# Optimization experiments

Measured on AMD Instinct MI355X. Metric: run time of the kernel, lower is better.

The kernel has to match this reference:

```python
import jax, jax.numpy as jnp
import numpy as np

N, D, H, DATT, C, NCLS = 20000, 1024, 512, 256, 10, 4

def setup_inputs() -> dict:
    key = jax.random.key(0)
    ks = jax.random.split(key, 20)
    s = lambda fan_in: 1.0 / np.sqrt(fan_in)
    u = lambda k, shape, fan_in: jax.random.uniform(k, shape, jnp.float32, -s(fan_in), s(fan_in))
    inp = {
        'x': jax.random.normal(ks[0], (N, D), jnp.float32),
        'cluster_id': jax.random.randint(ks[1], (N,), 0, C),
        # per-cluster expert MLP (phi_i): Linear(D,H)+ReLU, Linear(H,H)+ReLU (dropout=identity in eval)
        'W1': u(ks[2], (C, D, H), D), 'b1': u(ks[3], (C, H), D),
        'W2': u(ks[4], (C, H, H), H), 'b2': u(ks[5], (C, H), H),
        # attention_net: Linear(H,H)+ReLU then gated attention (L=H, D=DATT, n_classes=1)
        'fc_W': u(ks[6], (H, H), H), 'fc_b': u(ks[7], (H,), H),
        'Wa': u(ks[8], (H, DATT), H), 'ba': u(ks[9], (DATT,), H),
        'Wb': u(ks[10], (H, DATT), H), 'bb': u(ks[11], (DATT,), H),
        'Wc': u(ks[12], (DATT, 1), DATT), 'bc': u(ks[13], (1,), DATT),
        # rho: Linear(H, DATT)+ReLU
        'rho_W': u(ks[14], (H, DATT), H), 'rho_b': u(ks[15], (DATT,), H),
        # classifier
        'cls_W': u(ks[16], (DATT, NCLS), DATT), 'cls_b': u(ks[17], (NCLS,), DATT),
    }
    return inp

def reference(x, cluster_id, W1, b1, W2, b2, fc_W, fc_b, Wa, ba, Wb, bb, Wc, bc, rho_W, rho_b, cls_W, cls_b):
    # --- per-cluster expert MLPs, vectorized over clusters (no python loop over data) ---
    # h1: [C, N, H] = ReLU(x @ W1_c + b1_c) for every cluster c
    h1 = jax.nn.relu(jnp.einsum('nd,cdh->cnh', x, W1) + b1[:, None, :])
    h2 = jax.nn.relu(jnp.einsum('cnh,chk->cnk', h1, W2) + b2[:, None, :])
    # masked mean-pool per cluster (AdaptiveAvgPool1d(1) over the cluster's tokens)
    mask = (cluster_id[None, :] == jnp.arange(C)[:, None]).astype(h2.dtype)  # [C, N]
    counts = jnp.maximum(mask.sum(axis=1), 1.0)                               # empty cluster -> zeros
    h_cluster = jnp.einsum('cn,cnh->ch', mask, h2) / counts[:, None]          # [C, H]
    # --- attention net: fc + gated attention ---
    h = jax.nn.relu(h_cluster @ fc_W + fc_b)                                  # [C, H]
    a = jnp.tanh(h @ Wa + ba)
    b = jax.nn.sigmoid(h @ Wb + bb)
    A = ((a * b) @ Wc + bc).T                                                 # [1, C]
    A = jax.nn.softmax(A, axis=1)
    h_path = A @ h                                                            # [1, H]
    hr = jax.nn.relu(h_path @ rho_W + rho_b)[0]                               # [DATT] (squeeze)
    logits = (hr @ cls_W + cls_b)[None, :]                                    # [1, NCLS]
    Y_prob = jax.nn.softmax(logits, axis=1)
    Y_hat = jnp.argmax(logits, axis=1, keepdims=True)
    return (logits, Y_prob, Y_hat)
```

## Files before the change

### kernel.cpp

```cpp
#include <hip/hip_runtime.h>
#include <hip/hip_bf16.h>
#include <stdint.h>

#define NT 20000
#define DIM 1024
#define HID 512
#define DATT_N 256
#define NCLUS 10
#define NCLS_N 4
#define NRT 157
#define NBS 79

typedef __bf16 bf16;
typedef __attribute__((ext_vector_type(8))) __bf16 bf16x8;
typedef __attribute__((ext_vector_type(4))) float f32x4;

__device__ __forceinline__ void gload_lds16(const void* g, void* l) {
  __builtin_amdgcn_global_load_lds(
      (const __attribute__((address_space(1))) unsigned int*)g,
      (__attribute__((address_space(3))) unsigned int*)l, 16, 0, 0);
}


__global__ void zero_pool(float* pool) {
  int i = blockIdx.x * 256 + threadIdx.x;
  if (i < NCLUS * HID) pool[i] = 0.f;
}

__global__ __launch_bounds__(256) void hist_kernel(const int* __restrict__ cid,
                                                   int* __restrict__ blkcnt) {
  __shared__ int wcnt[4][16];
  int tid = threadIdx.x;
  int lane = tid & 63, w = tid >> 6;
  int n = blockIdx.x * 256 + tid;
  int mycid = (n < NT) ? cid[n] : -1;
#pragma unroll
  for (int c = 0; c < NCLUS; ++c) {
    unsigned long long m = __ballot(mycid == c);
    if (lane == c) wcnt[w][c] = __popcll(m);
  }
  __syncthreads();
  if (tid < NCLUS)
    blkcnt[blockIdx.x * NCLUS + tid] =
        wcnt[0][tid] + wcnt[1][tid] + wcnt[2][tid] + wcnt[3][tid];
}

__global__ void prefix_kernel(const int* __restrict__ blkcnt, int* __restrict__ blkbase,
                              int* __restrict__ cnt, int* __restrict__ offs) {
  int c = threadIdx.x;
  if (c < NCLUS) {
    int run = 0;
    for (int b = 0; b < NBS; ++b) {
      blkbase[b * NCLUS + c] = run;
      run += blkcnt[b * NCLUS + c];
    }
    cnt[c] = run;
  }
  __syncthreads();
  if (c == 0) {
    int a = 0;
    for (int i = 0; i < NCLUS; ++i) { offs[i] = a; a += cnt[i]; }
    offs[NCLUS] = a;
  }
}

__global__ __launch_bounds__(256) void scatter2_kernel(
    const int* __restrict__ cid, const int* __restrict__ blkbase,
    const int* __restrict__ offs, int* __restrict__ order) {
  __shared__ int wcnt[4][16];
  __shared__ int wbase[4][16];
  int tid = threadIdx.x;
  int lane = tid & 63, w = tid >> 6;
  int n = blockIdx.x * 256 + tid;
  int mycid = (n < NT) ? cid[n] : -1;
  unsigned long long lmask = (lane == 63) ? ~0ull >> 1 : (1ull << lane) - 1;
  int myrank = 0;
#pragma unroll
  for (int c = 0; c < NCLUS; ++c) {
    unsigned long long m = __ballot(mycid == c);
    if (mycid == c) myrank = __popcll(m & lmask);
    if (lane == c) wcnt[w][c] = __popcll(m);
  }
  __syncthreads();
  if (tid < NCLUS) {
    int pre = blkbase[blockIdx.x * NCLUS + tid];
#pragma unroll
    for (int ww = 0; ww < 4; ++ww) { wbase[ww][tid] = pre; pre += wcnt[ww][tid]; }
  }
  __syncthreads();
  if (n < NT) order[offs[mycid] + wbase[w][mycid] + myrank] = n;
}

__global__ void gather_cast(const float* __restrict__ x, const int* __restrict__ order,
                            bf16* __restrict__ xs) {
  int t = blockIdx.x * 256 + threadIdx.x;
  int row = t >> 7;
  if (row >= NT) return;
  int col = (t & 127) << 3;
  const f32x4* p = (const f32x4*)(x + (size_t)order[row] * DIM + col);
  f32x4 u = p[0], v = p[1];
  bf16x8 w;
  w[0] = (bf16)u[0]; w[1] = (bf16)u[1]; w[2] = (bf16)u[2]; w[3] = (bf16)u[3];
  w[4] = (bf16)v[0]; w[5] = (bf16)v[1]; w[6] = (bf16)v[2]; w[7] = (bf16)v[3];
  *(bf16x8*)(xs + (size_t)row * DIM + col) = w;
}

__global__ void transpose_cast(const float* __restrict__ src, bf16* __restrict__ dst,
                               int R, int Cc) {
  __shared__ float t[32][33];
  int b = blockIdx.z;
  int i0 = blockIdx.y * 32, j0 = blockIdx.x * 32;
  const float* s = src + (size_t)b * R * Cc;
  bf16* d = dst + (size_t)b * R * Cc;
  int tx = threadIdx.x & 31, ty = threadIdx.x >> 5;
#pragma unroll
  for (int yy = 0; yy < 32; yy += 8)
    t[ty + yy][tx] = s[(size_t)(i0 + ty + yy) * Cc + (j0 + tx)];
  __syncthreads();
#pragma unroll
  for (int yy = 0; yy < 32; yy += 8)
    d[(size_t)(j0 + ty + yy) * R + (i0 + tx)] = (bf16)t[tx][ty + yy];
}

__device__ __forceinline__ bool decode_grp(int d, int& c, int& rt, int& j) {
  int x8 = d & 7, s = d >> 3;
  int g = (s >> 2) * 8 + x8;
  if (g >= NRT * NCLUS) return false;
  j = s & 3;
  c = g / NRT;
  rt = g - c * NRT;
  return true;
}


__global__ __launch_bounds__(256, 2) void gemm1_kernel(
    const bf16* __restrict__ xs, const bf16* __restrict__ w1t, const float* __restrict__ b1,
    const int* __restrict__ offs, const int* __restrict__ cnt, bf16* __restrict__ h1) {
  int c, rt, j;
  if (!decode_grp(blockIdx.x, c, rt, j)) return;
  int cntc = cnt[c];
  int row0 = rt * 128;
  if (row0 >= cntc) return;
  int seg = offs[c];
  int n0 = j * 128;

  __shared__ bf16 Als[128 * 64];
  __shared__ bf16 Bls[128 * 64];

  int tid = threadIdx.x;
  int lane = tid & 63, wid = tid >> 6;
  int wr = wid >> 1, wc = wid & 1;

  const bf16* aptr[4]; int aoff[4];
  const bf16* bptr[4]; int boff[4];
#pragma unroll
  for (int i = 0; i < 4; ++i) {
    int chunk = i * 4 + wid;
    int r = chunk * 8 + (lane >> 3);
    int kk = (lane & 7) << 3;
    int ar = seg + row0 + r; if (ar > NT - 1) ar = NT - 1;
    aptr[i] = xs + (size_t)ar * DIM + kk;
    aoff[i] = chunk * 512;
    bptr[i] = w1t + (size_t)(c * HID + n0 + r) * DIM + kk;
    boff[i] = chunk * 512;
  }

  f32x4 acc[4][4];
#pragma unroll
  for (int m = 0; m < 4; m++)
#pragma unroll
    for (int n = 0; n < 4; n++) acc[m][n] = {0.f, 0.f, 0.f, 0.f};

  for (int k0 = 0; k0 < DIM; k0 += 64) {
#pragma unroll
    for (int i = 0; i < 4; ++i) gload_lds16(aptr[i] + k0, &Als[aoff[i]]);
#pragma unroll
    for (int i = 0; i < 4; ++i) gload_lds16(bptr[i] + k0, &Bls[boff[i]]);
    __syncthreads();
#pragma unroll
    for (int ks = 0; ks < 2; ++ks) {
      int ko = ks * 32 + ((lane >> 4) << 3);
      bf16x8 a[4], b[4];
#pragma unroll
      for (int m = 0; m < 4; m++)
        a[m] = *(const bf16x8*)(&Als[(wr * 64 + m * 16 + (lane & 15)) * 64 + ko]);
#pragma unroll
      for (int n = 0; n < 4; n++)
        b[n] = *(const bf16x8*)(&Bls[(wc * 64 + n * 16 + (lane & 15)) * 64 + ko]);
#pragma unroll
      for (int m = 0; m < 4; m++)
#pragma unroll
        for (int n = 0; n < 4; n++)
          acc[m][n] = __builtin_amdgcn_mfma_f32_16x16x32_bf16(a[m], b[n], acc[m][n], 0, 0, 0);
    }
    __syncthreads();
  }

  int valid = cntc - row0; if (valid > 128) valid = 128;
#pragma unroll
  for (int n = 0; n < 4; n++) {
    int col = n0 + wc * 64 + n * 16 + (lane & 15);
    float bias = b1[c * HID + col];
#pragma unroll
    for (int m = 0; m < 4; m++) {
      int rbase = wr * 64 + m * 16 + ((lane >> 4) << 2);
#pragma unroll
      for (int e = 0; e < 4; e++) {
        int r = rbase + e;
        if (r < valid) {
          float v = acc[m][n][e] + bias;
          h1[(size_t)(seg + row0 + r) * HID + col] = (bf16)(v > 0.f ? v : 0.f);
        }
      }
    }
  }
}


__global__ __launch_bounds__(256, 2) void gemm2_kernel(
    const bf16* __restrict__ h1, const bf16* __restrict__ w2t, const float* __restrict__ b2,
    const int* __restrict__ offs, const int* __restrict__ cnt, float* __restrict__ pool) {
  int c, rt, j;
  if (!decode_grp(blockIdx.x, c, rt, j)) return;
  int cntc = cnt[c];
  int row0 = rt * 128;
  if (row0 >= cntc) return;
  int seg = offs[c];
  int n0 = j * 128;
  int valid = cntc - row0; if (valid > 128) valid = 128;

  __shared__ bf16 Als[128 * 64];
  __shared__ bf16 Bls[128 * 64];

  int tid = threadIdx.x;
  int lane = tid & 63, wid = tid >> 6;
  int wr = wid >> 1, wc = wid & 1;

  const bf16* aptr[4]; int aoff[4];
  const bf16* bptr[4]; int boff[4];
#pragma unroll
  for (int i = 0; i < 4; ++i) {
    int chunk = i * 4 + wid;
    int r = chunk * 8 + (lane >> 3);
    int kk = (lane & 7) << 3;
    int ar = seg + row0 + r; if (ar > NT - 1) ar = NT - 1;
    aptr[i] = h1 + (size_t)ar * HID + kk;
    aoff[i] = chunk * 512;
    bptr[i] = w2t + (size_t)(c * HID + n0 + r) * HID + kk;
    boff[i] = chunk * 512;
  }

  f32x4 acc[4][4];
#pragma unroll
  for (int m = 0; m < 4; m++)
#pragma unroll
    for (int n = 0; n < 4; n++) acc[m][n] = {0.f, 0.f, 0.f, 0.f};

  for (int k0 = 0; k0 < HID; k0 += 64) {
#pragma unroll
    for (int i = 0; i < 4; ++i) gload_lds16(aptr[i] + k0, &Als[aoff[i]]);
#pragma unroll
    for (int i = 0; i < 4; ++i) gload_lds16(bptr[i] + k0, &Bls[boff[i]]);
    __syncthreads();
#pragma unroll
    for (int ks = 0; ks < 2; ++ks) {
      int ko = ks * 32 + ((lane >> 4) << 3);
      bf16x8 a[4], b[4];
#pragma unroll
      for (int m = 0; m < 4; m++)
        a[m] = *(const bf16x8*)(&Als[(wr * 64 + m * 16 + (lane & 15)) * 64 + ko]);
#pragma unroll
      for (int n = 0; n < 4; n++)
        b[n] = *(const bf16x8*)(&Bls[(wc * 64 + n * 16 + (lane & 15)) * 64 + ko]);
#pragma unroll
      for (int m = 0; m < 4; m++)
#pragma unroll
        for (int n = 0; n < 4; n++)
          acc[m][n] = __builtin_amdgcn_mfma_f32_16x16x32_bf16(a[m], b[n], acc[m][n], 0, 0, 0);
    }
    __syncthreads();
  }

#pragma unroll
  for (int n = 0; n < 4; n++) {
    int col = n0 + wc * 64 + n * 16 + (lane & 15);
    float bias = b2[c * HID + col];
    float s = 0.f;
#pragma unroll
    for (int m = 0; m < 4; m++) {
      int rbase = wr * 64 + m * 16 + ((lane >> 4) << 2);
#pragma unroll
      for (int e = 0; e < 4; e++) {
        if (rbase + e < valid) {
          float v = acc[m][n][e] + bias;
          s += (v > 0.f ? v : 0.f);
        }
      }
    }
    s += __shfl_xor(s, 16);
    s += __shfl_xor(s, 32);
    if (lane < 16) atomicAdd(&pool[c * HID + n0 + wc * 64 + n * 16 + lane], s);
  }
}


__global__ __launch_bounds__(256) void tail_fc(
    const float* __restrict__ pool, const int* __restrict__ cnt,
    const float* __restrict__ fcW, const float* __restrict__ fcb,
    float* __restrict__ hbuf) {
  int c = blockIdx.x >> 3;
  int jt = blockIdx.x & 7;
  __shared__ float hc[HID];
  __shared__ float red[4][64];
  int tid = threadIdx.x;
  float inv = 1.f / fmaxf((float)cnt[c], 1.f);
  for (int k = tid; k < HID; k += 256) hc[k] = pool[c * HID + k] * inv;
  __syncthreads();
  int jl = tid & 63, kg = tid >> 6;
  int j = jt * 64 + jl;
  float s = 0.f;
#pragma unroll 4
  for (int k = kg * 128; k < kg * 128 + 128; ++k) s += hc[k] * fcW[(size_t)k * HID + j];
  red[kg][jl] = s;
  __syncthreads();
  if (kg == 0) {
    float v = red[0][jl] + red[1][jl] + red[2][jl] + red[3][jl] + fcb[j];
    hbuf[c * HID + j] = fmaxf(v, 0.f);
  }
}

__global__ __launch_bounds__(1024) void tail_att(
    const float* __restrict__ hbuf,
    const float* __restrict__ Wa, const float* __restrict__ ba,
    const float* __restrict__ Wb, const float* __restrict__ bb,
    const float* __restrict__ Wc, const float* __restrict__ bc,
    float* __restrict__ score) {
  int c = blockIdx.x;
  __shared__ float h[HID];
  __shared__ float ra[4][DATT_N];
  __shared__ float rb[4][DATT_N];
  __shared__ float sc[DATT_N];
  int tid = threadIdx.x;
  for (int k = tid; k < HID; k += 1024) h[k] = hbuf[c * HID + k];
  __syncthreads();
  int jl = tid & 255, kg = tid >> 8;
  float sa = 0.f, sb = 0.f;
#pragma unroll 4
  for (int k = kg * 128; k < kg * 128 + 128; ++k) {
    float hv = h[k];
    sa += hv * Wa[(size_t)k * DATT_N + jl];
    sb += hv * Wb[(size_t)k * DATT_N + jl];
  }
  ra[kg][jl] = sa;
  rb[kg][jl] = sb;
  __syncthreads();
  if (kg == 0) {
    float va = ra[0][jl] + ra[1][jl] + ra[2][jl] + ra[3][jl] + ba[jl];
    float vb = rb[0][jl] + rb[1][jl] + rb[2][jl] + rb[3][jl] + bb[jl];
    float av = tanhf(va);
    float bv = 1.f / (1.f + expf(-vb));
    sc[jl] = av * bv * Wc[jl];
  }
  __syncthreads();
  for (int s2 = 128; s2 > 0; s2 >>= 1) {
    if (tid < s2) sc[tid] += sc[tid + s2];
    __syncthreads();
  }
  if (tid == 0) score[c] = sc[0] + bc[0];
}

__global__ __launch_bounds__(1024) void tail_fin(
    const float* __restrict__ score, const float* __restrict__ hbuf,
    const float* __restrict__ rhoW, const float* __restrict__ rhob,
    const float* __restrict__ clsW, const float* __restrict__ clsb,
    float* __restrict__ out) {
  __shared__ float Asm[NCLUS];
  __shared__ float hp[HID];
  __shared__ float rr[4][DATT_N];
  __shared__ float hr[DATT_N];
  __shared__ float lg[NCLS_N];
  int tid = threadIdx.x;
  if (tid == 0) {
    float mx = -1e30f;
    for (int c = 0; c < NCLUS; c++) mx = fmaxf(mx, score[c]);
    float sum = 0.f, e[NCLUS];
    for (int c = 0; c < NCLUS; c++) { e[c] = expf(score[c] - mx); sum += e[c]; }
    for (int c = 0; c < NCLUS; c++) Asm[c] = e[c] / sum;
  }
  __syncthreads();
  if (tid < HID) {
    float s = 0.f;
#pragma unroll
    for (int c = 0; c < NCLUS; c++) s += Asm[c] * hbuf[c * HID + tid];
    hp[tid] = s;
  }
  __syncthreads();
  int jl = tid & 255, kg = tid >> 8;
  float s = 0.f;
#pragma unroll 4
  for (int k = kg * 128; k < kg * 128 + 128; ++k) s += hp[k] * rhoW[(size_t)k * DATT_N + jl];
  rr[kg][jl] = s;
  __syncthreads();
  if (kg == 0) hr[jl] = fmaxf(rr[0][jl] + rr[1][jl] + rr[2][jl] + rr[3][jl] + rhob[jl], 0.f);
  __syncthreads();
  if (tid < NCLS_N * 64) {
    int t = tid >> 6, l = tid & 63;
    float cs = 0.f;
    for (int j = l; j < DATT_N; j += 64) cs += hr[j] * clsW[j * NCLS_N + t];
#pragma unroll
    for (int w = 32; w > 0; w >>= 1) cs += __shfl_xor(cs, w);
    if (l == 0) lg[t] = cs + clsb[t];
  }
  __syncthreads();
  if (tid == 0) {
    float mx = lg[0];
    int am = 0;
    for (int t = 1; t < NCLS_N; t++) if (lg[t] > mx) { mx = lg[t]; am = t; }
    float sum = 0.f, e[NCLS_N];
    for (int t = 0; t < NCLS_N; t++) { e[t] = expf(lg[t] - mx); sum += e[t]; }
    for (int t = 0; t < NCLS_N; t++) {
      out[t] = lg[t];
      out[NCLS_N + t] = e[t] / sum;
    }
    out[2 * NCLS_N] = (float)am;
  }
}


extern "C" void kernel_launch(void* const* d_in, const int* in_sizes, int n_in,
                              void* d_out, int out_size, void* d_ws, size_t ws_size,
                              hipStream_t stream) {
  const float* x    = (const float*)d_in[0];
  const int*   cid  = (const int*)d_in[1];
  const float* W1   = (const float*)d_in[2];
  const float* b1   = (const float*)d_in[3];
  const float* W2   = (const float*)d_in[4];
  const float* b2   = (const float*)d_in[5];
  const float* fcW  = (const float*)d_in[6];
  const float* fcb  = (const float*)d_in[7];
  const float* Wa   = (const float*)d_in[8];
  const float* ba   = (const float*)d_in[9];
  const float* Wb   = (const float*)d_in[10];
  const float* bb   = (const float*)d_in[11];
  const float* Wc   = (const float*)d_in[12];
  const float* bc   = (const float*)d_in[13];
  const float* rhoW = (const float*)d_in[14];
  const float* rhob = (const float*)d_in[15];
  const float* clsW = (const float*)d_in[16];
  const float* clsb = (const float*)d_in[17];
  float* out = (float*)d_out;

  char* ws = (char*)d_ws;
  int*   cnt     = (int*)(ws + 0);
  int*   offs    = (int*)(ws + 64);
  float* score   = (float*)(ws + 128);
  int*   blkcnt  = (int*)(ws + 256);
  int*   blkbase = (int*)(ws + 256 + 4096);
  int*   order   = (int*)(ws + 256 + 8192);
  float* pool    = (float*)(ws + 256 + 8192 + 80000);
  float* hbuf    = (float*)(ws + 256 + 8192 + 80000 + NCLUS * HID * 4);
  size_t o = 256 + 8192 + 80000 + 2ull * NCLUS * HID * 4;
  o = (o + 255) & ~(size_t)255;
  bf16* w1t = (bf16*)(ws + o); o += (size_t)NCLUS * HID * DIM * 2;
  bf16* w2t = (bf16*)(ws + o); o += (size_t)NCLUS * HID * HID * 2;
  bf16* h1  = (bf16*)(ws + o); o += (size_t)NT * HID * 2;
  bf16* xs  = (bf16*)(ws + o); o += (size_t)NT * DIM * 2;

  zero_pool<<<dim3((NCLUS * HID + 255) / 256), dim3(256), 0, stream>>>(pool);
  hist_kernel<<<dim3(NBS), dim3(256), 0, stream>>>(cid, blkcnt);
  prefix_kernel<<<dim3(1), dim3(64), 0, stream>>>(blkcnt, blkbase, cnt, offs);
  scatter2_kernel<<<dim3(NBS), dim3(256), 0, stream>>>(cid, blkbase, offs, order);
  gather_cast<<<dim3(NT * 128 / 256), dim3(256), 0, stream>>>(x, order, xs);
  transpose_cast<<<dim3(HID / 32, DIM / 32, NCLUS), dim3(256), 0, stream>>>(W1, w1t, DIM, HID);
  transpose_cast<<<dim3(HID / 32, HID / 32, NCLUS), dim3(256), 0, stream>>>(W2, w2t, HID, HID);

  int nblk = 8 * ((NRT * NCLUS + 7) / 8) * 4;
  gemm1_kernel<<<dim3(nblk), dim3(256), 0, stream>>>(xs, w1t, b1, offs, cnt, h1);
  gemm2_kernel<<<dim3(nblk), dim3(256), 0, stream>>>(h1, w2t, b2, offs, cnt, pool);

  tail_fc<<<dim3(NCLUS * 8), dim3(256), 0, stream>>>(pool, cnt, fcW, fcb, hbuf);
  tail_att<<<dim3(NCLUS), dim3(1024), 0, stream>>>(hbuf, Wa, ba, Wb, bb, Wc, bc, score);
  tail_fin<<<dim3(1), dim3(1024), 0, stream>>>(score, hbuf, rhoW, rhob, clsW, clsb, out);
}
```

Before: 146.6 us.

## Double-buffer LDS tiles and prefetch the next K-tile in both expert GEMMs

Both grouped GEMM kernels now use two LDS buffers for the A and B tiles. The global-to-LDS loads for K-tile t+1 are issued right after tile t's fragments are read into registers, before that tile's MFMAs run. This halves the barriers per iteration and is meant to hide global load latency behind matrix compute. In exchange, LDS per block doubles to 64KB, and more fragment registers are held live, which could put pressure on the 2-blocks-per-CU occupancy target.

```diff
diff --git a/kernel.cpp b/kernel.cpp
--- a/kernel.cpp
+++ b/kernel.cpp
@@ -144,8 +144,8 @@
   int seg = offs[c];
   int n0 = j * 128;
 
-  __shared__ bf16 Als[128 * 64];
-  __shared__ bf16 Bls[128 * 64];
+  __shared__ bf16 Als[2][128 * 64];
+  __shared__ bf16 Bls[2][128 * 64];
 
   int tid = threadIdx.x;
   int lane = tid & 63, wid = tid >> 6;
@@ -171,29 +171,43 @@
 #pragma unroll
     for (int n = 0; n < 4; n++) acc[m][n] = {0.f, 0.f, 0.f, 0.f};
 
-  for (int k0 = 0; k0 < DIM; k0 += 64) {
-#pragma unroll
-    for (int i = 0; i < 4; ++i) gload_lds16(aptr[i] + k0, &Als[aoff[i]]);
-#pragma unroll
-    for (int i = 0; i < 4; ++i) gload_lds16(bptr[i] + k0, &Bls[boff[i]]);
+#pragma unroll
+  for (int i = 0; i < 4; ++i) gload_lds16(aptr[i], &Als[0][aoff[i]]);
+#pragma unroll
+  for (int i = 0; i < 4; ++i) gload_lds16(bptr[i], &Bls[0][boff[i]]);
+
+  const int NKT = DIM / 64;
+#pragma unroll 2
+  for (int t = 0; t < NKT; ++t) {
     __syncthreads();
+    const bf16* Ab = &Als[t & 1][0];
+    const bf16* Bb = &Bls[t & 1][0];
+    bf16x8 a[2][4], b[2][4];
 #pragma unroll
     for (int ks = 0; ks < 2; ++ks) {
       int ko = ks * 32 + ((lane >> 4) << 3);
-      bf16x8 a[4], b[4];
 #pragma unroll
       for (int m = 0; m < 4; m++)
-        a[m] = *(const bf16x8*)(&Als[(wr * 64 + m * 16 + (lane & 15)) * 64 + ko]);
+        a[ks][m] = *(const bf16x8*)(&Ab[(wr * 64 + m * 16 + (lane & 15)) * 64 + ko]);
 #pragma unroll
       for (int n = 0; n < 4; n++)
-        b[n] = *(const bf16x8*)(&Bls[(wc * 64 + n * 16 + (lane & 15)) * 64 + ko]);
+        b[ks][n] = *(const bf16x8*)(&Bb[(wc * 64 + n * 16 + (lane & 15)) * 64 + ko]);
+    }
+    if (t + 1 < NKT) {
+      int k0 = (t + 1) * 64;
+      int nb = (t + 1) & 1;
+#pragma unroll
+      for (int i = 0; i < 4; ++i) gload_lds16(aptr[i] + k0, &Als[nb][aoff[i]]);
+#pragma unroll
+      for (int i = 0; i < 4; ++i) gload_lds16(bptr[i] + k0, &Bls[nb][boff[i]]);
+    }
+#pragma unroll
+    for (int ks = 0; ks < 2; ++ks)
 #pragma unroll
       for (int m = 0; m < 4; m++)
 #pragma unroll
         for (int n = 0; n < 4; n++)
-          acc[m][n] = __builtin_amdgcn_mfma_f32_16x16x32_bf16(a[m], b[n], acc[m][n], 0, 0, 0);
-    }
-    __syncthreads();
+          acc[m][n] = __builtin_amdgcn_mfma_f32_16x16x32_bf16(a[ks][m], b[ks][n], acc[m][n], 0, 0, 0);
   }
 
   int valid = cntc - row0; if (valid > 128) valid = 128;
@@ -229,8 +243,8 @@
   int n0 = j * 128;
   int valid = cntc - row0; if (valid > 128) valid = 128;
 
-  __shared__ bf16 Als[128 * 64];
-  __shared__ bf16 Bls[128 * 64];
+  __shared__ bf16 Als[2][128 * 64];
+  __shared__ bf16 Bls[2][128 * 64];
 
   int tid = threadIdx.x;
   int lane = tid & 63, wid = tid >> 6;
@@ -256,29 +270,43 @@
 #pragma unroll
     for (int n = 0; n < 4; n++) acc[m][n] = {0.f, 0.f, 0.f, 0.f};
 
-  for (int k0 = 0; k0 < HID; k0 += 64) {
-#pragma unroll
-    for (int i = 0; i < 4; ++i) gload_lds16(aptr[i] + k0, &Als[aoff[i]]);
-#pragma unroll
-    for (int i = 0; i < 4; ++i) gload_lds16(bptr[i] + k0, &Bls[boff[i]]);
+#pragma unroll
+  for (int i = 0; i < 4; ++i) gload_lds16(aptr[i], &Als[0][aoff[i]]);
+#pragma unroll
+  for (int i = 0; i < 4; ++i) gload_lds16(bptr[i], &Bls[0][boff[i]]);
+
+  const int NKT = HID / 64;
+#pragma unroll 2
+  for (int t = 0; t < NKT; ++t) {
     __syncthreads();
+    const bf16* Ab = &Als[t & 1][0];
+    const bf16* Bb = &Bls[t & 1][0];
+    bf16x8 a[2][4], b[2][4];
 #pragma unroll
     for (int ks = 0; ks < 2; ++ks) {
       int ko = ks * 32 + ((lane >> 4) << 3);
-      bf16x8 a[4], b[4];
 #pragma unroll
       for (int m = 0; m < 4; m++)
-        a[m] = *(const bf16x8*)(&Als[(wr * 64 + m * 16 + (lane & 15)) * 64 + ko]);
+        a[ks][m] = *(const bf16x8*)(&Ab[(wr * 64 + m * 16 + (lane & 15)) * 64 + ko]);
 #pragma unroll
       for (int n = 0; n < 4; n++)
-        b[n] = *(const bf16x8*)(&Bls[(wc * 64 + n * 16 + (lane & 15)) * 64 + ko]);
+        b[ks][n] = *(const bf16x8*)(&Bb[(wc * 64 + n * 16 + (lane & 15)) * 64 + ko]);
+    }
+    if (t + 1 < NKT) {
+      int k0 = (t + 1) * 64;
+      int nb = (t + 1) & 1;
+#pragma unroll
+      for (int i = 0; i < 4; ++i) gload_lds16(aptr[i] + k0, &Als[nb][aoff[i]]);
+#pragma unroll
+      for (int i = 0; i < 4; ++i) gload_lds16(bptr[i] + k0, &Bls[nb][boff[i]]);
+    }
+#pragma unroll
+    for (int ks = 0; ks < 2; ++ks)
 #pragma unroll
       for (int m = 0; m < 4; m++)
 #pragma unroll
         for (int n = 0; n < 4; n++)
-          acc[m][n] = __builtin_amdgcn_mfma_f32_16x16x32_bf16(a[m], b[n], acc[m][n], 0, 0, 0);
-    }
-    __syncthreads();
+          acc[m][n] = __builtin_amdgcn_mfma_f32_16x16x32_bf16(a[ks][m], b[ks][n], acc[m][n], 0, 0, 0);
   }
 
 #pragma unroll
```

Measured after the change: 163.3 us. 11.4% more time.

## Shrink GEMM tiles to 64x128 with 2 waves and merge setup kernels

Applied to the files above, without the earlier changes.

The two grouped GEMMs move from 128x128 tiles with 4 waves to 64x128 tiles with 2 waves per block. Each wave now computes 32x128, and launch bounds are raised to 3 blocks per CU. The smaller row tiles cut padding waste on each cluster's last tile and double the block count for better CU fill, but B-tile reuse per block drops. Separately, zero_pool, the histogram and both weight transposes are merged into one setup launch to remove launch overhead.

```diff
diff --git a/kernel.cpp b/kernel.cpp
--- a/kernel.cpp
+++ b/kernel.cpp
@@ -8,8 +8,8 @@
 #define DATT_N 256
 #define NCLUS 10
 #define NCLS_N 4
-#define NRT 157
 #define NBS 79
+#define NRT2 313
 
 typedef __bf16 bf16;
 typedef __attribute__((ext_vector_type(8))) __bf16 bf16x8;
@@ -22,27 +22,58 @@
 }
 
 
-__global__ void zero_pool(float* pool) {
-  int i = blockIdx.x * 256 + threadIdx.x;
-  if (i < NCLUS * HID) pool[i] = 0.f;
-}
-
-__global__ __launch_bounds__(256) void hist_kernel(const int* __restrict__ cid,
-                                                   int* __restrict__ blkcnt) {
+__device__ __forceinline__ void transpose_body(const float* __restrict__ s,
+                                               bf16* __restrict__ d, int R, int Cc,
+                                               int i0, int j0, float (*t)[33]) {
+  int tx = threadIdx.x & 31, ty = threadIdx.x >> 5;
+#pragma unroll
+  for (int yy = 0; yy < 32; yy += 8)
+    t[ty + yy][tx] = s[(size_t)(i0 + ty + yy) * Cc + (j0 + tx)];
+  __syncthreads();
+#pragma unroll
+  for (int yy = 0; yy < 32; yy += 8)
+    d[(size_t)(j0 + ty + yy) * R + (i0 + tx)] = (bf16)t[tx][ty + yy];
+}
+
+#define ZPB ((NCLUS * HID + 255) / 256)
+#define TW1B (16 * 32 * NCLUS)
+#define TW2B (16 * 16 * NCLUS)
+
+__global__ __launch_bounds__(256) void setup_kernel(
+    const int* __restrict__ cid, int* __restrict__ blkcnt, float* __restrict__ pool,
+    const float* __restrict__ W1, bf16* __restrict__ w1t,
+    const float* __restrict__ W2, bf16* __restrict__ w2t) {
+  __shared__ float t[32][33];
   __shared__ int wcnt[4][16];
-  int tid = threadIdx.x;
-  int lane = tid & 63, w = tid >> 6;
-  int n = blockIdx.x * 256 + tid;
-  int mycid = (n < NT) ? cid[n] : -1;
-#pragma unroll
-  for (int c = 0; c < NCLUS; ++c) {
-    unsigned long long m = __ballot(mycid == c);
-    if (lane == c) wcnt[w][c] = __popcll(m);
-  }
-  __syncthreads();
-  if (tid < NCLUS)
-    blkcnt[blockIdx.x * NCLUS + tid] =
-        wcnt[0][tid] + wcnt[1][tid] + wcnt[2][tid] + wcnt[3][tid];
+  int b = blockIdx.x;
+  int tid = threadIdx.x;
+  if (b < NBS) {
+    int lane = tid & 63, w = tid >> 6;
+    int n = b * 256 + tid;
+    int mycid = (n < NT) ? cid[n] : -1;
+#pragma unroll
+    for (int c = 0; c < NCLUS; ++c) {
+      unsigned long long m = __ballot(mycid == c);
+      if (lane == c) wcnt[w][c] = __popcll(m);
+    }
+    __syncthreads();
+    if (tid < NCLUS)
+      blkcnt[b * NCLUS + tid] =
+          wcnt[0][tid] + wcnt[1][tid] + wcnt[2][tid] + wcnt[3][tid];
+  } else if (b < NBS + ZPB) {
+    int i = (b - NBS) * 256 + tid;
+    if (i < NCLUS * HID) pool[i] = 0.f;
+  } else if (b < NBS + ZPB + TW1B) {
+    int bb = b - NBS - ZPB;
+    int z = bb >> 9, r = bb & 511, y = r >> 4, x = r & 15;
+    transpose_body(W1 + (size_t)z * DIM * HID, w1t + (size_t)z * DIM * HID,
+                   DIM, HID, y * 32, x * 32, t);
+  } else {
+    int bb = b - NBS - ZPB - TW1B;
+    int z = bb >> 8, r = bb & 255, y = r >> 4, x = r & 15;
+    transpose_body(W2 + (size_t)z * HID * HID, w2t + (size_t)z * HID * HID,
+                   HID, HID, y * 32, x * 32, t);
+  }
 }
 
 __global__ void prefix_kernel(const int* __restrict__ blkcnt, int* __restrict__ blkbase,
@@ -105,105 +136,93 @@
   *(bf16x8*)(xs + (size_t)row * DIM + col) = w;
 }
 
-__global__ void transpose_cast(const float* __restrict__ src, bf16* __restrict__ dst,
-                               int R, int Cc) {
-  __shared__ float t[32][33];
-  int b = blockIdx.z;
-  int i0 = blockIdx.y * 32, j0 = blockIdx.x * 32;
-  const float* s = src + (size_t)b * R * Cc;
-  bf16* d = dst + (size_t)b * R * Cc;
-  int tx = threadIdx.x & 31, ty = threadIdx.x >> 5;
-#pragma unroll
-  for (int yy = 0; yy < 32; yy += 8)
-    t[ty + yy][tx] = s[(size_t)(i0 + ty + yy) * Cc + (j0 + tx)];
-  __syncthreads();
-#pragma unroll
-  for (int yy = 0; yy < 32; yy += 8)
-    d[(size_t)(j0 + ty + yy) * R + (i0 + tx)] = (bf16)t[tx][ty + yy];
-}
-
-__device__ __forceinline__ bool decode_grp(int d, int& c, int& rt, int& j) {
+__device__ __forceinline__ bool decode_grp2(int d, int& c, int& rt, int& j) {
   int x8 = d & 7, s = d >> 3;
   int g = (s >> 2) * 8 + x8;
-  if (g >= NRT * NCLUS) return false;
+  if (g >= NRT2 * NCLUS) return false;
   j = s & 3;
-  c = g / NRT;
-  rt = g - c * NRT;
+  c = g / NRT2;
+  rt = g - c * NRT2;
   return true;
 }
 
 
-__global__ __launch_bounds__(256, 2) void gemm1_kernel(
+__global__ __launch_bounds__(128, 3) void gemm1_kernel(
     const bf16* __restrict__ xs, const bf16* __restrict__ w1t, const float* __restrict__ b1,
     const int* __restrict__ offs, const int* __restrict__ cnt, bf16* __restrict__ h1) {
   int c, rt, j;
-  if (!decode_grp(blockIdx.x, c, rt, j)) return;
+  if (!decode_grp2(blockIdx.x, c, rt, j)) return;
   int cntc = cnt[c];
-  int row0 = rt * 128;
+  int row0 = rt * 64;
   if (row0 >= cntc) return;
   int seg = offs[c];
   int n0 = j * 128;
 
-  __shared__ bf16 Als[128 * 64];
+  __shared__ bf16 Als[64 * 64];
   __shared__ bf16 Bls[128 * 64];
 
   int tid = threadIdx.x;
-  int lane = tid & 63, wid = tid >> 6;
-  int wr = wid >> 1, wc = wid & 1;
+  int lane = tid & 63, w = tid >> 6;
 
   const bf16* aptr[4]; int aoff[4];
-  const bf16* bptr[4]; int boff[4];
+  const bf16* bptr[8]; int boff[8];
 #pragma unroll
   for (int i = 0; i < 4; ++i) {
-    int chunk = i * 4 + wid;
-    int r = chunk * 8 + (lane >> 3);
+    int ch = i * 2 + w;
+    int r = ch * 8 + (lane >> 3);
     int kk = (lane & 7) << 3;
     int ar = seg + row0 + r; if (ar > NT - 1) ar = NT - 1;
     aptr[i] = xs + (size_t)ar * DIM + kk;
-    aoff[i] = chunk * 512;
+    aoff[i] = ch * 512;
+  }
+#pragma unroll
+  for (int i = 0; i < 8; ++i) {
+    int ch = i * 2 + w;
+    int r = ch * 8 + (lane >> 3);
+    int kk = (lane & 7) << 3;
     bptr[i] = w1t + (size_t)(c * HID + n0 + r) * DIM + kk;
-    boff[i] = chunk * 512;
-  }
-
-  f32x4 acc[4][4];
-#pragma unroll
-  for (int m = 0; m < 4; m++)
-#pragma unroll
-    for (int n = 0; n < 4; n++) acc[m][n] = {0.f, 0.f, 0.f, 0.f};
+    boff[i] = ch * 512;
+  }
+
+  f32x4 acc[2][8];
+#pragma unroll
+  for (int m = 0; m < 2; m++)
+#pragma unroll
+    for (int n = 0; n < 8; n++) acc[m][n] = {0.f, 0.f, 0.f, 0.f};
 
   for (int k0 = 0; k0 < DIM; k0 += 64) {
 #pragma unroll
     for (int i = 0; i < 4; ++i) gload_lds16(aptr[i] + k0, &Als[aoff[i]]);
 #pragma unroll
-    for (int i = 0; i < 4; ++i) gload_lds16(bptr[i] + k0, &Bls[boff[i]]);
+    for (int i = 0; i < 8; ++i) gload_lds16(bptr[i] + k0, &Bls[boff[i]]);
     __syncthreads();
 #pragma unroll
     for (int ks = 0; ks < 2; ++ks) {
       int ko = ks * 32 + ((lane >> 4) << 3);
-      bf16x8 a[4], b[4];
-#pragma unroll
-      for (int m = 0; m < 4; m++)
-        a[m] = *(const bf16x8*)(&Als[(wr * 64 + m * 16 + (lane & 15)) * 64 + ko]);
-#pragma unroll
-      for (int n = 0; n < 4; n++)
-        b[n] = *(const bf16x8*)(&Bls[(wc * 64 + n * 16 + (lane & 15)) * 64 + ko]);
-#pragma unroll
-      for (int m = 0; m < 4; m++)
-#pragma unroll
-        for (int n = 0; n < 4; n++)
+      bf16x8 a[2], b[8];
+#pragma unroll
+      for (int m = 0; m < 2; m++)
+        a[m] = *(const bf16x8*)(&Als[(w * 32 + m * 16 + (lane & 15)) * 64 + ko]);
+#pragma unroll
+      for (int n = 0; n < 8; n++)
+        b[n] = *(const bf16x8*)(&Bls[(n * 16 + (lane & 15)) * 64 + ko]);
+#pragma unroll
+      for (int m = 0; m < 2; m++)
+#pragma unroll
+        for (int n = 0; n < 8; n++)
           acc[m][n] = __builtin_amdgcn_mfma_f32_16x16x32_bf16(a[m], b[n], acc[m][n], 0, 0, 0);
     }
     __syncthreads();
   }
 
-  int valid = cntc - row0; if (valid > 128) valid = 128;
-#pragma unroll
-  for (int n = 0; n < 4; n++) {
-    int col = n0 + wc * 64 + n * 16 + (lane & 15);
+  int valid = cntc - row0; if (valid > 64) valid = 64;
+#pragma unroll
+  for (int n = 0; n < 8; n++) {
+    int col = n0 + n * 16 + (lane & 15);
     float bias = b1[c * HID + col];
 #pragma unroll
-    for (int m = 0; m < 4; m++) {
-      int rbase = wr * 64 + m * 16 + ((lane >> 4) << 2);
+    for (int m = 0; m < 2; m++) {
+      int rbase = w * 32 + m * 16 + ((lane >> 4) << 2);
 #pragma unroll
       for (int e = 0; e < 4; e++) {
         int r = rbase + e;
@@ -217,78 +236,83 @@
 }
 
 
-__global__ __launch_bounds__(256, 2) void gemm2_kernel(
+__global__ __launch_bounds__(128, 3) void gemm2_kernel(
     const bf16* __restrict__ h1, const bf16* __restrict__ w2t, const float* __restrict__ b2,
     const int* __restrict__ offs, const int* __restrict__ cnt, float* __restrict__ pool) {
   int c, rt, j;
-  if (!decode_grp(blockIdx.x, c, rt, j)) return;
+  if (!decode_grp2(blockIdx.x, c, rt, j)) return;
   int cntc = cnt[c];
-  int row0 = rt * 128;
+  int row0 = rt * 64;
   if (row0 >= cntc) return;
   int seg = offs[c];
   int n0 = j * 128;
-  int valid = cntc - row0; if (valid > 128) valid = 128;
-
-  __shared__ bf16 Als[128 * 64];
+  int valid = cntc - row0; if (valid > 64) valid = 64;
+
+  __shared__ bf16 Als[64 * 64];
   __shared__ bf16 Bls[128 * 64];
 
   int tid = threadIdx.x;
-  int lane = tid & 63, wid = tid >> 6;
-  int wr = wid >> 1, wc = wid & 1;
+  int lane = tid & 63, w = tid >> 6;
 
   const bf16* aptr[4]; int aoff[4];
-  const bf16* bptr[4]; int boff[4];
+  const bf16* bptr[8]; int boff[8];
 #pragma unroll
   for (int i = 0; i < 4; ++i) {
-    int chunk = i * 4 + wid;
-    int r = chunk * 8 + (lane >> 3);
+    int ch = i * 2 + w;
+    int r = ch * 8 + (lane >> 3);
     int kk = (lane & 7) << 3;
     int ar = seg + row0 + r; if (ar > NT - 1) ar = NT - 1;
     aptr[i] = h1 + (size_t)ar * HID + kk;
-    aoff[i] = chunk * 512;
+    aoff[i] = ch * 512;
+  }
+#pragma unroll
+  for (int i = 0; i < 8; ++i) {
+    int ch = i * 2 + w;
+    int r = ch * 8 + (lane >> 3);
+    int kk = (lane & 7) << 3;
     bptr[i] = w2t + (size_t)(c * HID + n0 + r) * HID + kk;
-    boff[i] = chunk * 512;
-  }
-
-  f32x4 acc[4][4];
-#pragma unroll
-  for (int m = 0; m < 4; m++)
-#pragma unroll
-    for (int n = 0; n < 4; n++) acc[m][n] = {0.f, 0.f, 0.f, 0.f};
+    boff[i] = ch * 512;
+  }
+
+  f32x4 acc[2][8];
+#pragma unroll
+  for (int m = 0; m < 2; m++)
+#pragma unroll
+    for (int n = 0; n < 8; n++) acc[m][n] = {0.f, 0.f, 0.f, 0.f};
 
   for (int k0 = 0; k0 < HID; k0 += 64) {
 #pragma unroll
     for (int i = 0; i < 4; ++i) gload_lds16(aptr[i] + k0, &Als[aoff[i]]);
 #pragma unroll
-    for (int i = 0; i < 4; ++i) gload_lds16(bptr[i] + k0, &Bls[boff[i]]);
+    for (int i = 0; i < 8; ++i) gload_lds16(bptr[i] + k0, &Bls[boff[i]]);
     __syncthreads();
 #pragma unroll
     for (int ks = 0; ks < 2; ++ks) {
       int ko = ks * 32 + ((lane >> 4) << 3);
-      bf16x8 a[4], b[4];
-#pragma unroll
-      for (int m = 0; m < 4; m++)
-        a[m] = *(const bf16x8*)(&Als[(wr * 64 + m * 16 + (lane & 15)) * 64 + ko]);
-#pragma unroll
-      for (int n = 0; n < 4; n++)
-        b[n] = *(const bf16x8*)(&Bls[(wc * 64 + n * 16 + (lane & 15)) * 64 + ko]);
-#pragma unroll
-      for (int m = 0; m < 4; m++)
-#pragma unroll
-        for (int n = 0; n < 4; n++)
+      bf16x8 a[2], b[8];
+#pragma unroll
+      for (int m = 0; m < 2; m++)
+        a[m] = *(const bf16x8*)(&Als[(w * 32 + m * 16 + (lane & 15)) * 64 + ko]);
+#pragma unroll
+      for (int n = 0; n < 8; n++)
+        b[n] = *(const bf16x8*)(&Bls[(n * 16 + (lane & 15)) * 64 + ko]);
+#pragma unroll
+      for (int m = 0; m < 2; m++)
+#pragma unroll
+        for (int n = 0; n < 8; n++)
           acc[m][n] = __builtin_amdgcn_mfma_f32_16x16x32_bf16(a[m], b[n], acc[m][n], 0, 0, 0);
     }
     __syncthreads();
   }
 
 #pragma unroll
-  for (int n = 0; n < 4; n++) {
-    int col = n0 + wc * 64 + n * 16 + (lane & 15);
+  for (int n = 0; n < 8; n++) {
+    int col = n0 + n * 16 + (lane & 15);
     float bias = b2[c * HID + col];
     float s = 0.f;
 #pragma unroll
-    for (int m = 0; m < 4; m++) {
-      int rbase = wr * 64 + m * 16 + ((lane >> 4) << 2);
+    for (int m = 0; m < 2; m++) {
+      int rbase = w * 32 + m * 16 + ((lane >> 4) << 2);
 #pragma unroll
       for (int e = 0; e < 4; e++) {
         if (rbase + e < valid) {
@@ -299,7 +323,7 @@
     }
     s += __shfl_xor(s, 16);
     s += __shfl_xor(s, 32);
-    if (lane < 16) atomicAdd(&pool[c * HID + n0 + wc * 64 + n * 16 + lane], s);
+    if (lane < 16) atomicAdd(&pool[c * HID + col], s);
   }
 }
 
@@ -466,17 +490,15 @@
   bf16* h1  = (bf16*)(ws + o); o += (size_t)NT * HID * 2;
   bf16* xs  = (bf16*)(ws + o); o += (size_t)NT * DIM * 2;
 
-  zero_pool<<<dim3((NCLUS * HID + 255) / 256), dim3(256), 0, stream>>>(pool);
-  hist_kernel<<<dim3(NBS), dim3(256), 0, stream>>>(cid, blkcnt);
+  setup_kernel<<<dim3(NBS + ZPB + TW1B + TW2B), dim3(256), 0, stream>>>(
+      cid, blkcnt, pool, W1, w1t, W2, w2t);
   prefix_kernel<<<dim3(1), dim3(64), 0, stream>>>(blkcnt, blkbase, cnt, offs);
   scatter2_kernel<<<dim3(NBS), dim3(256), 0, stream>>>(cid, blkbase, offs, order);
   gather_cast<<<dim3(NT * 128 / 256), dim3(256), 0, stream>>>(x, order, xs);
-  transpose_cast<<<dim3(HID / 32, DIM / 32, NCLUS), dim3(256), 0, stream>>>(W1, w1t, DIM, HID);
-  transpose_cast<<<dim3(HID / 32, HID / 32, NCLUS), dim3(256), 0, stream>>>(W2, w2t, HID, HID);
-
-  int nblk = 8 * ((NRT * NCLUS + 7) / 8) * 4;
-  gemm1_kernel<<<dim3(nblk), dim3(256), 0, stream>>>(xs, w1t, b1, offs, cnt, h1);
-  gemm2_kernel<<<dim3(nblk), dim3(256), 0, stream>>>(h1, w2t, b2, offs, cnt, pool);
+
+  int nblk = 8 * ((NRT2 * NCLUS + 7) / 8) * 4;
+  gemm1_kernel<<<dim3(nblk), dim3(128), 0, stream>>>(xs, w1t, b1, offs, cnt, h1);
+  gemm2_kernel<<<dim3(nblk), dim3(128), 0, stream>>>(h1, w2t, b2, offs, cnt, pool);
 
   tail_fc<<<dim3(NCLUS * 8), dim3(256), 0, stream>>>(pool, cnt, fcW, fcb, hbuf);
   tail_att<<<dim3(NCLUS), dim3(1024), 0, stream>>>(hbuf, Wa, ba, Wb, bb, Wc, bc, score);
```

Result: no change. 147.3 us (+0.5%).

## Fuse setup kernels, fold prefix scan into scatter, swizzle GEMM LDS tiles

Applied to the files above, without the earlier changes.

Merges the histogram, pool zeroing and both weight transpose-casts into one setup kernel whose block ranges select the role. The transpose is rewritten to use vectorized 16-byte loads and stores. The prefix scan now runs redundantly inside each scatter block, which removes the separate prefix kernel and the blkbase buffer. Both GEMMs apply an XOR swizzle on the k-chunk for the LDS staging and the fragment reads to cut LDS bank conflicts. The intent is fewer launches and cheaper shared-memory access, at the cost of every scatter block re-reading all block counts.

```diff
diff --git a/kernel.cpp b/kernel.cpp
--- a/kernel.cpp
+++ b/kernel.cpp
@@ -8,8 +8,8 @@
 #define DATT_N 256
 #define NCLUS 10
 #define NCLS_N 4
+#define NBS 79
 #define NRT 157
-#define NBS 79
 
 typedef __bf16 bf16;
 typedef __attribute__((ext_vector_type(8))) __bf16 bf16x8;
@@ -22,56 +22,98 @@
 }
 
 
-__global__ void zero_pool(float* pool) {
-  int i = blockIdx.x * 256 + threadIdx.x;
-  if (i < NCLUS * HID) pool[i] = 0.f;
-}
-
-__global__ __launch_bounds__(256) void hist_kernel(const int* __restrict__ cid,
-                                                   int* __restrict__ blkcnt) {
+#define ZPB 20
+#define TW1B (32 * 4 * NCLUS)
+#define TW2B (16 * 4 * NCLUS)
+
+__device__ __forceinline__ void tr_body(const float* __restrict__ s, bf16* __restrict__ d,
+                                        int R, int Cc, int i0, int j0, float (*t)[128]) {
+  int tid = threadIdx.x;
+  int cr = tid >> 5;
+  int cc4 = (tid & 31) << 2;
+#pragma unroll
+  for (int yy = 0; yy < 32; yy += 8)
+    *(f32x4*)&t[yy + cr][cc4] = *(const f32x4*)&s[(size_t)(i0 + yy + cr) * Cc + j0 + cc4];
+  __syncthreads();
+  int col = tid >> 1, h = (tid & 1) << 4;
+  bf16 tmp[16];
+#pragma unroll
+  for (int k = 0; k < 16; ++k) tmp[k] = (bf16)t[h + k][col];
+  *(bf16x8*)&d[(size_t)(j0 + col) * R + i0 + h] = *(bf16x8*)&tmp[0];
+  *(bf16x8*)&d[(size_t)(j0 + col) * R + i0 + h + 8] = *(bf16x8*)&tmp[8];
+}
+
+__global__ __launch_bounds__(256) void setup_kernel(
+    const int* __restrict__ cid, int* __restrict__ blkcnt, float* __restrict__ pool,
+    const float* __restrict__ W1, bf16* __restrict__ w1t,
+    const float* __restrict__ W2, bf16* __restrict__ w2t) {
+  __shared__ float t[32][128];
   __shared__ int wcnt[4][16];
-  int tid = threadIdx.x;
-  int lane = tid & 63, w = tid >> 6;
-  int n = blockIdx.x * 256 + tid;
-  int mycid = (n < NT) ? cid[n] : -1;
-#pragma unroll
-  for (int c = 0; c < NCLUS; ++c) {
-    unsigned long long m = __ballot(mycid == c);
-    if (lane == c) wcnt[w][c] = __popcll(m);
-  }
-  __syncthreads();
-  if (tid < NCLUS)
-    blkcnt[blockIdx.x * NCLUS + tid] =
-        wcnt[0][tid] + wcnt[1][tid] + wcnt[2][tid] + wcnt[3][tid];
-}
-
-__global__ void prefix_kernel(const int* __restrict__ blkcnt, int* __restrict__ blkbase,
-                              int* __restrict__ cnt, int* __restrict__ offs) {
-  int c = threadIdx.x;
-  if (c < NCLUS) {
-    int run = 0;
-    for (int b = 0; b < NBS; ++b) {
-      blkbase[b * NCLUS + c] = run;
-      run += blkcnt[b * NCLUS + c];
-    }
-    cnt[c] = run;
-  }
-  __syncthreads();
-  if (c == 0) {
-    int a = 0;
-    for (int i = 0; i < NCLUS; ++i) { offs[i] = a; a += cnt[i]; }
-    offs[NCLUS] = a;
-  }
-}
-
-__global__ __launch_bounds__(256) void scatter2_kernel(
-    const int* __restrict__ cid, const int* __restrict__ blkbase,
-    const int* __restrict__ offs, int* __restrict__ order) {
+  int b = blockIdx.x;
+  int tid = threadIdx.x;
+  if (b < NBS) {
+    int lane = tid & 63, w = tid >> 6;
+    int n = b * 256 + tid;
+    int mycid = (n < NT) ? cid[n] : -1;
+#pragma unroll
+    for (int c = 0; c < NCLUS; ++c) {
+      unsigned long long m = __ballot(mycid == c);
+      if (lane == c) wcnt[w][c] = __popcll(m);
+    }
+    __syncthreads();
+    if (tid < NCLUS)
+      blkcnt[b * NCLUS + tid] =
+          wcnt[0][tid] + wcnt[1][tid] + wcnt[2][tid] + wcnt[3][tid];
+  } else if (b < NBS + ZPB) {
+    int i = (b - NBS) * 256 + tid;
+    if (i < NCLUS * HID) pool[i] = 0.f;
+  } else if (b < NBS + ZPB + TW1B) {
+    int bb = b - NBS - ZPB;
+    int z = bb >> 7, r = bb & 127, rt = r >> 2, ct = r & 3;
+    tr_body(W1 + (size_t)z * DIM * HID, w1t + (size_t)z * DIM * HID,
+            DIM, HID, rt * 32, ct * 128, t);
+  } else {
+    int bb = b - NBS - ZPB - TW1B;
+    int z = bb >> 6, r = bb & 63, rt = r >> 2, ct = r & 3;
+    tr_body(W2 + (size_t)z * HID * HID, w2t + (size_t)z * HID * HID,
+            HID, HID, rt * 32, ct * 128, t);
+  }
+}
+
+
+__global__ __launch_bounds__(256) void scatter_kernel(
+    const int* __restrict__ cid, const int* __restrict__ blkcnt,
+    int* __restrict__ cnt, int* __restrict__ offs, int* __restrict__ order) {
+  __shared__ int sbase[16];
+  __shared__ int scnt[16];
+  __shared__ int soffs[16];
   __shared__ int wcnt[4][16];
   __shared__ int wbase[4][16];
   int tid = threadIdx.x;
   int lane = tid & 63, w = tid >> 6;
-  int n = blockIdx.x * 256 + tid;
+  int bx = blockIdx.x;
+  if (tid < NCLUS) {
+    int base = 0, run = 0;
+    for (int b = 0; b < NBS; ++b) {
+      int v = blkcnt[b * NCLUS + tid];
+      if (b < bx) base += v;
+      run += v;
+    }
+    sbase[tid] = base;
+    scnt[tid] = run;
+  }
+  __syncthreads();
+  if (tid == 0) {
+    int a = 0;
+    for (int i = 0; i < NCLUS; ++i) { soffs[i] = a; a += scnt[i]; }
+    soffs[NCLUS] = a;
+  }
+  __syncthreads();
+  if (bx == 0 && tid <= NCLUS) {
+    if (tid < NCLUS) cnt[tid] = scnt[tid];
+    offs[tid] = soffs[tid];
+  }
+  int n = bx * 256 + tid;
   int mycid = (n < NT) ? cid[n] : -1;
   unsigned long long lmask = (lane == 63) ? ~0ull >> 1 : (1ull << lane) - 1;
   int myrank = 0;
@@ -83,13 +125,14 @@
   }
   __syncthreads();
   if (tid < NCLUS) {
-    int pre = blkbase[blockIdx.x * NCLUS + tid];
+    int pre = sbase[tid];
 #pragma unroll
     for (int ww = 0; ww < 4; ++ww) { wbase[ww][tid] = pre; pre += wcnt[ww][tid]; }
   }
   __syncthreads();
-  if (n < NT) order[offs[mycid] + wbase[w][mycid] + myrank] = n;
-}
+  if (n < NT) order[soffs[mycid] + wbase[w][mycid] + myrank] = n;
+}
+
 
 __global__ void gather_cast(const float* __restrict__ x, const int* __restrict__ order,
                             bf16* __restrict__ xs) {
@@ -105,23 +148,6 @@
   *(bf16x8*)(xs + (size_t)row * DIM + col) = w;
 }
 
-__global__ void transpose_cast(const float* __restrict__ src, bf16* __restrict__ dst,
-                               int R, int Cc) {
-  __shared__ float t[32][33];
-  int b = blockIdx.z;
-  int i0 = blockIdx.y * 32, j0 = blockIdx.x * 32;
-  const float* s = src + (size_t)b * R * Cc;
-  bf16* d = dst + (size_t)b * R * Cc;
-  int tx = threadIdx.x & 31, ty = threadIdx.x >> 5;
-#pragma unroll
-  for (int yy = 0; yy < 32; yy += 8)
-    t[ty + yy][tx] = s[(size_t)(i0 + ty + yy) * Cc + (j0 + tx)];
-  __syncthreads();
-#pragma unroll
-  for (int yy = 0; yy < 32; yy += 8)
-    d[(size_t)(j0 + ty + yy) * R + (i0 + tx)] = (bf16)t[tx][ty + yy];
-}
-
 __device__ __forceinline__ bool decode_grp(int d, int& c, int& rt, int& j) {
   int x8 = d & 7, s = d >> 3;
   int g = (s >> 2) * 8 + x8;
@@ -150,6 +176,8 @@
   int tid = threadIdx.x;
   int lane = tid & 63, wid = tid >> 6;
   int wr = wid >> 1, wc = wid & 1;
+  int rx = lane & 7, hi = lane >> 4;
+  int kswz = ((lane & 7) ^ (lane >> 3)) << 3;
 
   const bf16* aptr[4]; int aoff[4];
   const bf16* bptr[4]; int boff[4];
@@ -157,11 +185,10 @@
   for (int i = 0; i < 4; ++i) {
     int chunk = i * 4 + wid;
     int r = chunk * 8 + (lane >> 3);
-    int kk = (lane & 7) << 3;
     int ar = seg + row0 + r; if (ar > NT - 1) ar = NT - 1;
-    aptr[i] = xs + (size_t)ar * DIM + kk;
+    aptr[i] = xs + (size_t)ar * DIM + kswz;
     aoff[i] = chunk * 512;
-    bptr[i] = w1t + (size_t)(c * HID + n0 + r) * DIM + kk;
+    bptr[i] = w1t + (size_t)(c * HID + n0 + r) * DIM + kswz;
     boff[i] = chunk * 512;
   }
 
@@ -179,7 +206,8 @@
     __syncthreads();
 #pragma unroll
     for (int ks = 0; ks < 2; ++ks) {
-      int ko = ks * 32 + ((lane >> 4) << 3);
+      int t16 = ks * 4 + hi;
+      int ko = ((t16 ^ rx) << 3);
       bf16x8 a[4], b[4];
 #pragma unroll
       for (int m = 0; m < 4; m++)
@@ -235,6 +263,8 @@
   int tid = threadIdx.x;
   int lane = tid & 63, wid = tid >> 6;
   int wr = wid >> 1, wc = wid & 1;
+  int rx = lane & 7, hi = lane >> 4;
+  int kswz = ((lane & 7) ^ (lane >> 3)) << 3;
 
   const bf16* aptr[4]; int aoff[4];
   const bf16* bptr[4]; int boff[4];
@@ -242,11 +272,10 @@
   for (int i = 0; i < 4; ++i) {
     int chunk = i * 4 + wid;
     int r = chunk * 8 + (lane >> 3);
-    int kk = (lane & 7) << 3;
     int ar = seg + row0 + r; if (ar > NT - 1) ar = NT - 1;
-    aptr[i] = h1 + (size_t)ar * HID + kk;
+    aptr[i] = h1 + (size_t)ar * HID + kswz;
     aoff[i] = chunk * 512;
-    bptr[i] = w2t + (size_t)(c * HID + n0 + r) * HID + kk;
+    bptr[i] = w2t + (size_t)(c * HID + n0 + r) * HID + kswz;
     boff[i] = chunk * 512;
   }
 
@@ -264,7 +293,8 @@
     __syncthreads();
 #pragma unroll
     for (int ks = 0; ks < 2; ++ks) {
-      int ko = ks * 32 + ((lane >> 4) << 3);
+      int t16 = ks * 4 + hi;
+      int ko = ((t16 ^ rx) << 3);
       bf16x8 a[4], b[4];
 #pragma unroll
       for (int m = 0; m < 4; m++)
@@ -455,24 +485,20 @@
   int*   offs    = (int*)(ws + 64);
   float* score   = (float*)(ws + 128);
   int*   blkcnt  = (int*)(ws + 256);
-  int*   blkbase = (int*)(ws + 256 + 4096);
-  int*   order   = (int*)(ws + 256 + 8192);
-  float* pool    = (float*)(ws + 256 + 8192 + 80000);
-  float* hbuf    = (float*)(ws + 256 + 8192 + 80000 + NCLUS * HID * 4);
-  size_t o = 256 + 8192 + 80000 + 2ull * NCLUS * HID * 4;
+  int*   order   = (int*)(ws + 256 + 4096);
+  float* pool    = (float*)(ws + 256 + 4096 + 80000);
+  float* hbuf    = (float*)(ws + 256 + 4096 + 80000 + NCLUS * HID * 4);
+  size_t o = 256 + 4096 + 80000 + 2ull * NCLUS * HID * 4;
   o = (o + 255) & ~(size_t)255;
   bf16* w1t = (bf16*)(ws + o); o += (size_t)NCLUS * HID * DIM * 2;
   bf16* w2t = (bf16*)(ws + o); o += (size_t)NCLUS * HID * HID * 2;
   bf16* h1  = (bf16*)(ws + o); o += (size_t)NT * HID * 2;
   bf16* xs  = (bf16*)(ws + o); o += (size_t)NT * DIM * 2;
 
-  zero_pool<<<dim3((NCLUS * HID + 255) / 256), dim3(256), 0, stream>>>(pool);
-  hist_kernel<<<dim3(NBS), dim3(256), 0, stream>>>(cid, blkcnt);
-  prefix_kernel<<<dim3(1), dim3(64), 0, stream>>>(blkcnt, blkbase, cnt, offs);
-  scatter2_kernel<<<dim3(NBS), dim3(256), 0, stream>>>(cid, blkbase, offs, order);
+  setup_kernel<<<dim3(NBS + ZPB + TW1B + TW2B), dim3(256), 0, stream>>>(
+      cid, blkcnt, pool, W1, w1t, W2, w2t);
+  scatter_kernel<<<dim3(NBS), dim3(256), 0, stream>>>(cid, blkcnt, cnt, offs, order);
   gather_cast<<<dim3(NT * 128 / 256), dim3(256), 0, stream>>>(x, order, xs);
-  transpose_cast<<<dim3(HID / 32, DIM / 32, NCLUS), dim3(256), 0, stream>>>(W1, w1t, DIM, HID);
-  transpose_cast<<<dim3(HID / 32, HID / 32, NCLUS), dim3(256), 0, stream>>>(W2, w2t, HID, HID);
 
   int nblk = 8 * ((NRT * NCLUS + 7) / 8) * 4;
   gemm1_kernel<<<dim3(nblk), dim3(256), 0, stream>>>(xs, w1t, b1, offs, cnt, h1);
```

Result: faster. 128.4 us (-12.4%).
